# Optimization experiments

Measured on AMD Instinct MI355X. Metric: run time of the kernel, lower is better.

Reference implementation:

```python
import jax, jax.numpy as jnp
import numpy as np

# Hyperparameters (must match init_kwargs)
B, S, D = 1, 4096, 1024
H, DK, DV = 16, 64, 64
G, W, R = 1, 23, 8          # global, window, random tokens
KSEL = 1 + R + W            # selected keys per non-global query


def setup_inputs() -> dict:
    key = jax.random.key(0)
    ks = jax.random.split(key, 8)
    scale = 0.02
    Q = jax.random.normal(ks[0], (B, S, D), dtype=jnp.float32)
    K = jax.random.normal(ks[1], (B, S, D), dtype=jnp.float32)
    V = jax.random.normal(ks[2], (B, S, D), dtype=jnp.float32)
    Wq = jax.random.normal(ks[3], (D, H * DK), dtype=jnp.float32) * scale
    Wk = jax.random.normal(ks[4], (D, H * DK), dtype=jnp.float32) * scale
    Wv = jax.random.normal(ks[5], (D, H * DV), dtype=jnp.float32) * scale
    Wo = jax.random.normal(ks[6], (H * DV, D), dtype=jnp.float32) * scale
    # BigBird-style index table: [global(=token 0), random, sliding window]
    n_ng = S - 2 * G
    base = jnp.arange(G, S - G)                                   # [n_ng]
    win = base[:, None] + jnp.arange(W)[None, :] - (W - 1) // 2   # [n_ng, W]
    win = jnp.clip(win, 0, S - 1)
    rnd = jax.random.randint(ks[7], (n_ng, R), 1, S)              # [n_ng, R]
    glb = jnp.zeros((n_ng, 1), dtype=jnp.int64)
    idx = jnp.concatenate([glb, rnd.astype(jnp.int64), win.astype(jnp.int64)], axis=1)  # [n_ng, KSEL]
    return {"Q": Q, "K": K, "V": V, "Wq": Wq, "Wk": Wk, "Wv": Wv, "Wo": Wo, "idx": idx}


def reference(Q, K, V, Wq, Wk, Wv, Wo, idx):
    b, s, _ = Q.shape
    g = G
    # Projections, split heads: [B,H,S,d]
    q = (Q @ Wq).reshape(b, s, H, DK).transpose(0, 2, 1, 3)
    k = (K @ Wk).reshape(b, s, H, DK).transpose(0, 2, 1, 3)
    v = (V @ Wv).reshape(b, s, H, DV).transpose(0, 2, 1, 3)
    scale = 1.0 / jnp.sqrt(jnp.asarray(DK, dtype=q.dtype))

    # --- dense global-token path: first g and last g queries attend to all keys ---
    gidx = jnp.concatenate([jnp.arange(g), jnp.arange(s - g, s)])  # [2g]
    q_g = q[:, :, gidx, :]                                          # [B,H,2g,dk]
    logits_g = jnp.einsum('bhgd,bhnd->bhgn', q_g, k) * scale
    prob_g = jax.nn.softmax(logits_g, axis=-1)
    out_g = jnp.einsum('bhgn,bhnd->bhgd', prob_g, v)                # [B,H,2g,dv]

    # --- sparse gather path for the remaining queries ---
    q_ng = q[:, :, g:s - g, :]                                      # [B,H,n_ng,dk]
    k_sel = k[:, :, idx, :]                                         # [B,H,n_ng,KSEL,dk]
    v_sel = v[:, :, idx, :]                                         # [B,H,n_ng,KSEL,dv]
    logits = jnp.einsum('bhnd,bhnkd->bhnk', q_ng, k_sel) * scale
    prob = jax.nn.softmax(logits, axis=-1)
    out_ng = jnp.einsum('bhnk,bhnkd->bhnd', prob, v_sel)            # [B,H,n_ng,dv]

    out = jnp.concatenate([out_g[:, :, :g], out_ng, out_g[:, :, g:]], axis=2)  # [B,H,S,dv]
    x = out.transpose(0, 2, 1, 3).reshape(b, s, H * DV)
    return x @ Wo
```

## Files before the change

### kernel.cpp

```cpp
#include <hip/hip_runtime.h>

typedef unsigned short u16;
typedef unsigned int u32;
typedef __bf16 bf16x8_t __attribute__((ext_vector_type(8)));
typedef float f32x4 __attribute__((ext_vector_type(4)));
typedef float f32x2 __attribute__((ext_vector_type(2)));
typedef u32 u32x4 __attribute__((ext_vector_type(4)));
typedef u16 u16x8 __attribute__((ext_vector_type(8)));

__device__ __forceinline__ float b2f(u16 u) {
  u32 x = ((u32)u) << 16; float f; __builtin_memcpy(&f, &x, 4); return f;
}
__device__ __forceinline__ u16 f2b(float f) {
  u32 x; __builtin_memcpy(&x, &f, 4);
  return (u16)((x + 0x8000u) >> 16);
}
__device__ __forceinline__ f32x2 up2(u32 w) {
  u32 lo = w << 16, hi = w & 0xffff0000u;
  float a, b; __builtin_memcpy(&a, &lo, 4); __builtin_memcpy(&b, &hi, 4);
  f32x2 r; r[0] = a; r[1] = b; return r;
}

__device__ __forceinline__ u16x8 ld8(const void* p, size_t off, int f32) {
  if (!f32) return *(const u16x8*)((const u16*)p + off);
  const u32* u = (const u32*)p + off;
  u32x4 a = *(const u32x4*)u;
  u32x4 b = *(const u32x4*)(u + 4);
  u16x8 r;
#pragma unroll
  for (int e = 0; e < 4; ++e) r[e] = (u16)((a[e] + 0x8000u) >> 16);
#pragma unroll
  for (int e = 0; e < 4; ++e) r[4 + e] = (u16)((b[e] + 0x8000u) >> 16);
  return r;
}

#if __has_builtin(__builtin_amdgcn_global_load_lds)
__device__ __forceinline__ void gl_lds16(const u16* g, u16* l, int lane) {
  (void)lane;
  __builtin_amdgcn_global_load_lds(
      (const __attribute__((address_space(1))) void*)g,
      (__attribute__((address_space(3))) void*)l, 16, 0, 0);
}
#else
__device__ __forceinline__ void gl_lds16(const u16* g, u16* l, int lane) {
  *(u16x8*)(l + lane * 8) = *(const u16x8*)g;
}
#endif

__device__ __forceinline__ int det_f32(const u32* qraw, int lane) {
  int c = 0;
#pragma unroll
  for (int p = 0; p < 8; ++p) {
    const int e = (qraw[p * 64 + lane] >> 7) & 0xFF;
    c += (e >= 100 && e <= 141);
  }
  for (int off = 32; off; off >>= 1) c += __shfl_xor(c, off);
  return c < 300;
}
__device__ __forceinline__ int det_i64(const int* iraw, int lane) {
  int nz = (lane < 16) ? (iraw[(lane + 1) * 32 + 1] != 0) : 0;
  return __ballot(nz) == 0ull;
}

__global__ __launch_bounds__(256) void prep(
    const void* Q, const void* K, const void* V,
    const void* W0, const void* W1, const void* W2, const void* W3,
    u16* d0, u16* d1, u16* d2, u16* d3,
    u16* Qb, u16* Kb, u16* Vb) {
  const int tx = threadIdx.x, ty = threadIdx.y;
  const int t = ty * 32 + tx;
  const int f32 = det_f32((const u32*)Q, t & 63);
  const int z = blockIdx.z;
  if (z >= 4) {
    if (!f32) return;
    const void* s; u16* d;
    switch (z - 4) {
      case 0: s = Q; d = Qb; break;
      case 1: s = K; d = Kb; break;
      default: s = V; d = Vb; break;
    }
    const size_t i = ((size_t)(blockIdx.y * 32 + blockIdx.x) * 256 + t) * 16;
    *(u16x8*)(d + i) = ld8(s, i, 1);
    *(u16x8*)(d + i + 8) = ld8(s, i + 8, 1);
    return;
  }
  const void* src; u16* dst;
  switch (z) {
    case 0: src = W0; dst = d0; break;
    case 1: src = W1; dst = d1; break;
    case 2: src = W2; dst = d2; break;
    default: src = W3; dst = d3; break;
  }
  __shared__ u16 tile[32][33];
  const int bx = blockIdx.x * 32, by = blockIdx.y * 32;
#pragma unroll
  for (int i = 0; i < 4; ++i) {
    const int off = (by + ty + i * 8) * 1024 + bx + tx;
    tile[ty + i * 8][tx] = f32 ? f2b(((const float*)src)[off]) : ((const u16*)src)[off];
  }
  __syncthreads();
#pragma unroll
  for (int i = 0; i < 4; ++i)
    dst[(bx + ty + i * 8) * 1024 + by + tx] = tile[tx][ty + i * 8];
}

template <int BM>
__device__ __forceinline__ void gemm_fast(const void* A, int a_f32,
                                          const u16* __restrict__ Bt,
                                          void* C, int c_f32) {
  constexpr int AI = BM / 64;
  __shared__ __align__(16) u16 As[BM * 32];
  __shared__ __align__(16) u16 Bs[128 * 32];
  const int t = threadIdx.x;
  const int lane = t & 63, w = t >> 6;
  const int bm = blockIdx.x * BM, bn = blockIdx.y * 128;
  const int lr = lane >> 2, lc = (lane & 3) * 8;
  const int wr = (w >> 1) * (BM / 2);
  const int wc = (w & 1) * 64;
  const int m16 = lane & 15, q4 = lane >> 4;
  f32x4 acc[BM / 32][4] = {};

  for (int k0 = 0; k0 < 1024; k0 += 32) {
    if (!a_f32) {
#pragma unroll
      for (int i = 0; i < AI; ++i)
        gl_lds16((const u16*)A + (size_t)(bm + w * 16 * AI + i * 16 + lr) * 1024 + k0 + lc,
                 &As[(w * 16 * AI + i * 16) * 32], lane);
    } else {
#pragma unroll
      for (int i = 0; i < AI; ++i)
        *(u16x8*)&As[(w * 16 * AI + i * 16 + lr) * 32 + lc] =
            ld8(A, (size_t)(bm + w * 16 * AI + i * 16 + lr) * 1024 + k0 + lc, 1);
    }
    gl_lds16(Bt + (size_t)(bn + w * 32 + lr) * 1024 + k0 + lc, &Bs[(w * 32) * 32], lane);
    gl_lds16(Bt + (size_t)(bn + w * 32 + 16 + lr) * 1024 + k0 + lc, &Bs[(w * 32 + 16) * 32], lane);
    __syncthreads();
    bf16x8_t af[BM / 32], bfr[4];
#pragma unroll
    for (int i = 0; i < BM / 32; ++i)
      af[i] = *(const bf16x8_t*)&As[(wr + i * 16 + m16) * 32 + q4 * 8];
#pragma unroll
    for (int j = 0; j < 4; ++j)
      bfr[j] = *(const bf16x8_t*)&Bs[(wc + j * 16 + m16) * 32 + q4 * 8];
#pragma unroll
    for (int i = 0; i < BM / 32; ++i)
#pragma unroll
      for (int j = 0; j < 4; ++j)
        acc[i][j] = __builtin_amdgcn_mfma_f32_16x16x32_bf16(af[i], bfr[j], acc[i][j], 0, 0, 0);
    __syncthreads();
  }
#pragma unroll
  for (int i = 0; i < BM / 32; ++i)
#pragma unroll
    for (int r = 0; r < 4; ++r) {
      const int row = bm + wr + i * 16 + q4 * 4 + r;
#pragma unroll
      for (int j = 0; j < 4; ++j) {
        const int col = bn + wc + j * 16 + m16;
        const float x = acc[i][j][r];
        if (c_f32) ((float*)C)[(size_t)row * 1024 + col] = x;
        else       ((u16*)C)[(size_t)row * 1024 + col] = f2b(x);
      }
    }
}

__global__ __launch_bounds__(256) void gemm_qkv(
    const void* Q, const void* K, const void* V,
    const u16* Qb, const u16* Kb, const u16* Vb,
    const u16* WqT, const u16* WkT, const u16* WvT,
    u16* q, u16* k, u16* v, int big) {
  const int f32 = det_f32((const u32*)Q, threadIdx.x & 63);
  const void* Araw; const u16* Ab; const u16* Bt; u16* Cp;
  switch (blockIdx.z) {
    case 0:  Araw = Q; Ab = Qb; Bt = WqT; Cp = q; break;
    case 1:  Araw = K; Ab = Kb; Bt = WkT; Cp = k; break;
    default: Araw = V; Ab = Vb; Bt = WvT; Cp = v; break;
  }
  if (big && f32) gemm_fast<128>(Ab, 0, Bt, Cp, 0);
  else            gemm_fast<128>(Araw, f32, Bt, Cp, 0);
}

__global__ __launch_bounds__(256) void gemm_out(
    const void* Qdet, const u16* A, const u16* WoT, void* C) {
  const int f32 = det_f32((const u32*)Qdet, threadIdx.x & 63);
  gemm_fast<64>(A, 0, WoT, C, f32);
}

__global__ __launch_bounds__(256) void attn(
    u16* qp, const u16* __restrict__ kp, const u16* __restrict__ vp,
    const int* __restrict__ idx, float* __restrict__ part) {
  const int t = threadIdx.x;
  __shared__ float ps[512];
  __shared__ int sidx[32];
  __shared__ float qh[64];
  __shared__ float lg[512];
  __shared__ float red[4];
  __shared__ float pvs[4][64];

  if (blockIdx.x < 256) {
    const int qi = blockIdx.x >> 7;
    const int h = (blockIdx.x >> 3) & 15;
    const int c = blockIdx.x & 7;
    const int s = qi ? 4095 : 0;
    if (t < 8) {
      u16x8 v = *(const u16x8*)(qp + (size_t)s * 1024 + h * 64 + t * 8);
#pragma unroll
      for (int e = 0; e < 8; ++e) qh[t * 8 + e] = b2f((u16)v[e]);
    }
    __syncthreads();
    float lv[2];
#pragma unroll
    for (int i = 0; i < 2; ++i) {
      const int n = c * 512 + t + i * 256;
      const u16* krow = kp + (size_t)n * 1024 + h * 64;
      float acc = 0.f;
#pragma unroll
      for (int cc = 0; cc < 8; ++cc) {
        u16x8 kv = *(const u16x8*)(krow + cc * 8);
#pragma unroll
        for (int e = 0; e < 8; ++e) acc += qh[cc * 8 + e] * b2f((u16)kv[e]);
      }
      lv[i] = acc * 0.125f;
    }
    float m2 = fmaxf(lv[0], lv[1]);
    for (int off = 32; off; off >>= 1) m2 = fmaxf(m2, __shfl_xor(m2, off));
    if ((t & 63) == 0) red[t >> 6] = m2;
    __syncthreads();
    const float gm = fmaxf(fmaxf(red[0], red[1]), fmaxf(red[2], red[3]));
    const float p0 = __expf(lv[0] - gm), p1 = __expf(lv[1] - gm);
    lg[t & 255] = p0;
    lg[t + 256] = p1;
    float sm = p0 + p1;
    for (int off = 32; off; off >>= 1) sm += __shfl_xor(sm, off);
    __syncthreads();
    if ((t & 63) == 0) red[t >> 6] = sm;
    __syncthreads();
    const float ssum = red[0] + red[1] + red[2] + red[3];
    const int d = t & 63, cc = t >> 6;
    float acc = 0.f;
    for (int i = 0; i < 128; ++i) {
      const int nl = cc * 128 + i;
      acc += lg[nl] * b2f(vp[(size_t)(c * 512 + nl) * 1024 + h * 64 + d]);
    }
    pvs[cc][d] = acc;
    __syncthreads();
    float* dst = part + ((size_t)(qi * 16 + h) * 8 + c) * 66;
    if (t == 0) { dst[0] = gm; dst[1] = ssum; }
    if (t < 64) dst[2 + t] = pvs[0][t] + pvs[1][t] + pvs[2][t] + pvs[3][t];
    return;
  }

  const int b = blockIdx.x - 256;
  int s0 = (b & 7) * 512 + (b >> 3);
  if (s0 >= 4094) s0 = 3583;
  const int s = s0 + 1;
  const int w = t >> 6, lane = t & 63;
  const int i64f = det_i64(idx, lane);
  const int jj = lane >> 3, dl = lane & 7;

  if (t >= 224) {
    const int j = t - 224;
    const size_t e = (size_t)(s - 1) * 32 + j;
    sidx[j] = i64f ? idx[2 * e] : idx[e];
  }

  f32x2 qreg[4][4];
#pragma unroll
  for (int hh = 0; hh < 4; ++hh) {
    const u32x4 qw = *(const u32x4*)(qp + (size_t)s * 1024 + (w * 4 + hh) * 64 + dl * 8);
#pragma unroll
    for (int c = 0; c < 4; ++c) qreg[hh][c] = up2(qw[c]);
  }
  __syncthreads();

#pragma unroll
  for (int p = 0; p < 16; ++p) {
    const int h = w * 4 + (p >> 2);
    const int j = (p & 3) * 8 + jj;
    const u32x4 kw = *(const u32x4*)(kp + (size_t)sidx[j] * 1024 + h * 64 + dl * 8);
    f32x2 a2 = {0.f, 0.f};
#pragma unroll
    for (int c = 0; c < 4; ++c)
      a2 = __builtin_elementwise_fma(up2(kw[c]), qreg[p >> 2][c], a2);
    float acc = a2[0] + a2[1];
    acc += __shfl_xor(acc, 1);
    acc += __shfl_xor(acc, 2);
    acc += __shfl_xor(acc, 4);
    if (dl == 0) ps[h * 32 + j] = acc * 0.125f;
  }
  __syncthreads();

  {
    const int h = t >> 4, jx = t & 15;
    const float v0 = ps[h * 32 + jx], v1 = ps[h * 32 + jx + 16];
    float mx = fmaxf(v0, v1);
    mx = fmaxf(mx, __shfl_xor(mx, 1));
    mx = fmaxf(mx, __shfl_xor(mx, 2));
    mx = fmaxf(mx, __shfl_xor(mx, 4));
    mx = fmaxf(mx, __shfl_xor(mx, 8));
    const float p0 = __expf(v0 - mx), p1 = __expf(v1 - mx);
    float sm = p0 + p1;
    sm += __shfl_xor(sm, 1);
    sm += __shfl_xor(sm, 2);
    sm += __shfl_xor(sm, 4);
    sm += __shfl_xor(sm, 8);
    const float r = 1.f / sm;
    ps[h * 32 + jx] = p0 * r;
    ps[h * 32 + jx + 16] = p1 * r;
  }
  __syncthreads();

  const int dc = lane & 7;
#pragma unroll
  for (int hp = 0; hp < 4; ++hp) {
    const int h = hp * 4 + w;
    f32x2 acc2[4] = {};
#pragma unroll
    for (int j0 = 0; j0 < 32; j0 += 8) {
      const int j = j0 + jj;
      const u32x4 vw = *(const u32x4*)(vp + (size_t)sidx[j] * 1024 + h * 64 + dc * 8);
      const float p = ps[h * 32 + j];
      const f32x2 pp = {p, p};
#pragma unroll
      for (int c = 0; c < 4; ++c)
        acc2[c] = __builtin_elementwise_fma(up2(vw[c]), pp, acc2[c]);
    }
#pragma unroll
    for (int c = 0; c < 4; ++c)
#pragma unroll
      for (int e = 0; e < 2; ++e) {
        acc2[c][e] += __shfl_xor(acc2[c][e], 8);
        acc2[c][e] += __shfl_xor(acc2[c][e], 16);
        acc2[c][e] += __shfl_xor(acc2[c][e], 32);
      }
    if (jj == 0) {
      u16x8 o;
#pragma unroll
      for (int c = 0; c < 4; ++c) {
        o[c * 2] = f2b(acc2[c][0]);
        o[c * 2 + 1] = f2b(acc2[c][1]);
      }
      *(u16x8*)(qp + (size_t)s * 1024 + h * 64 + dc * 8) = o;
    }
  }
}

__global__ void attn_glb_b(u16* __restrict__ qp, const float* __restrict__ part) {
  const int qi = blockIdx.x >> 4, h = blockIdx.x & 15;
  const int s = qi ? 4095 : 0;
  const int t = threadIdx.x;
  const float* p = part + ((size_t)(qi * 16 + h) * 8) * 66;
  float gm = -1e30f;
#pragma unroll
  for (int c = 0; c < 8; ++c) gm = fmaxf(gm, p[c * 66]);
  float S = 0.f, o = 0.f;
#pragma unroll
  for (int c = 0; c < 8; ++c) {
    const float w = __expf(p[c * 66] - gm);
    S += p[c * 66 + 1] * w;
    o += p[c * 66 + 2 + t] * w;
  }
  qp[(size_t)s * 1024 + h * 64 + t] = f2b(o / S);
}

extern "C" void kernel_launch(void* const* d_in, const int* in_sizes, int n_in,
                              void* d_out, int out_size, void* d_ws, size_t ws_size,
                              hipStream_t stream) {
  const void* Q  = d_in[0];
  const void* K  = d_in[1];
  const void* V  = d_in[2];
  const void* Wq = d_in[3];
  const void* Wk = d_in[4];
  const void* Wv = d_in[5];
  const void* Wo = d_in[6];
  const int* idx = (const int*)d_in[7];

  u16* WqT = (u16*)d_ws;
  u16* WkT = WqT + (1 << 20);
  u16* WvT = WkT + (1 << 20);
  u16* WoT = WvT + (1 << 20);
  u16* qp  = WoT + (1 << 20);
  u16* vp  = qp + (4 << 20);
  float* part = (float*)WkT;
  u16* kp = (u16*)d_out;
  u16* Qb = (u16*)((char*)d_ws + (24ull << 20) + 4096);
  u16* Kb = Qb + (4 << 20);
  u16* Vb = Kb + (4 << 20);
  const bool big = ws_size >= (48ull << 20) + 8192;

  prep<<<dim3(32, 32, big ? 7 : 4), dim3(32, 8), 0, stream>>>(
      Q, K, V, Wq, Wk, Wv, Wo, WqT, WkT, WvT, WoT, Qb, Kb, Vb);
  gemm_qkv<<<dim3(32, 8, 3), 256, 0, stream>>>(
      Q, K, V, Qb, Kb, Vb, WqT, WkT, WvT, qp, kp, vp, big ? 1 : 0);
  attn<<<4350, 256, 0, stream>>>(qp, kp, vp, idx, part);
  attn_glb_b<<<32, 64, 0, stream>>>(qp, part);
  gemm_out<<<dim3(64, 8), 256, 0, stream>>>(Q, qp, WoT, d_out);
}
```

Baseline: 225.0 us.

## Restructure attention kernel to wave-local work without shared memory or block barriers

The sparse-query path now keeps the gathered indices, logits and softmax probabilities in registers. Indices are broadcast with wave shuffles, which removes all LDS staging and __syncthreads calls. The global-token path is re-split so each wave handles 128 keys of one head with vectorized 16-byte K/V loads, replacing per-element V loads and block reductions. The partial-result layout grows to 32 chunks of 72 floats, and the combine kernel changes to match. The larger partial buffer must fit in the workspace, and the combine step now has more partial chunks to read.

```diff
diff --git a/kernel.cpp b/kernel.cpp
--- a/kernel.cpp
+++ b/kernel.cpp
@@ -190,63 +190,73 @@
     u16* qp, const u16* __restrict__ kp, const u16* __restrict__ vp,
     const int* __restrict__ idx, float* __restrict__ part) {
   const int t = threadIdx.x;
-  __shared__ float ps[512];
-  __shared__ int sidx[32];
-  __shared__ float qh[64];
-  __shared__ float lg[512];
-  __shared__ float red[4];
-  __shared__ float pvs[4][64];
+  const int w = t >> 6, lane = t & 63;
+  const int jj = lane >> 3, dl = lane & 7;
 
   if (blockIdx.x < 256) {
-    const int qi = blockIdx.x >> 7;
-    const int h = (blockIdx.x >> 3) & 15;
-    const int c = blockIdx.x & 7;
+    const int gw = blockIdx.x * 4 + w;
+    const int qi = gw >> 9, h = (gw >> 5) & 15, c = gw & 31;
     const int s = qi ? 4095 : 0;
-    if (t < 8) {
-      u16x8 v = *(const u16x8*)(qp + (size_t)s * 1024 + h * 64 + t * 8);
-#pragma unroll
-      for (int e = 0; e < 8; ++e) qh[t * 8 + e] = b2f((u16)v[e]);
-    }
-    __syncthreads();
-    float lv[2];
-#pragma unroll
-    for (int i = 0; i < 2; ++i) {
-      const int n = c * 512 + t + i * 256;
-      const u16* krow = kp + (size_t)n * 1024 + h * 64;
-      float acc = 0.f;
-#pragma unroll
-      for (int cc = 0; cc < 8; ++cc) {
-        u16x8 kv = *(const u16x8*)(krow + cc * 8);
-#pragma unroll
-        for (int e = 0; e < 8; ++e) acc += qh[cc * 8 + e] * b2f((u16)kv[e]);
-      }
-      lv[i] = acc * 0.125f;
-    }
-    float m2 = fmaxf(lv[0], lv[1]);
-    for (int off = 32; off; off >>= 1) m2 = fmaxf(m2, __shfl_xor(m2, off));
-    if ((t & 63) == 0) red[t >> 6] = m2;
-    __syncthreads();
-    const float gm = fmaxf(fmaxf(red[0], red[1]), fmaxf(red[2], red[3]));
-    const float p0 = __expf(lv[0] - gm), p1 = __expf(lv[1] - gm);
-    lg[t & 255] = p0;
-    lg[t + 256] = p1;
-    float sm = p0 + p1;
-    for (int off = 32; off; off >>= 1) sm += __shfl_xor(sm, off);
-    __syncthreads();
-    if ((t & 63) == 0) red[t >> 6] = sm;
-    __syncthreads();
-    const float ssum = red[0] + red[1] + red[2] + red[3];
-    const int d = t & 63, cc = t >> 6;
-    float acc = 0.f;
-    for (int i = 0; i < 128; ++i) {
-      const int nl = cc * 128 + i;
-      acc += lg[nl] * b2f(vp[(size_t)(c * 512 + nl) * 1024 + h * 64 + d]);
-    }
-    pvs[cc][d] = acc;
-    __syncthreads();
-    float* dst = part + ((size_t)(qi * 16 + h) * 8 + c) * 66;
-    if (t == 0) { dst[0] = gm; dst[1] = ssum; }
-    if (t < 64) dst[2 + t] = pvs[0][t] + pvs[1][t] + pvs[2][t] + pvs[3][t];
+    f32x2 qreg[4];
+    {
+      const u32x4 qw = *(const u32x4*)(qp + (size_t)s * 1024 + h * 64 + dl * 8);
+#pragma unroll
+      for (int cc = 0; cc < 4; ++cc) qreg[cc] = up2(qw[cc]);
+    }
+    float lre[16];
+#pragma unroll
+    for (int p = 0; p < 16; ++p) {
+      const int n = c * 128 + p * 8 + jj;
+      const u32x4 kw = *(const u32x4*)(kp + (size_t)n * 1024 + h * 64 + dl * 8);
+      f32x2 a2 = {0.f, 0.f};
+#pragma unroll
+      for (int cc = 0; cc < 4; ++cc)
+        a2 = __builtin_elementwise_fma(up2(kw[cc]), qreg[cc], a2);
+      float acc = a2[0] + a2[1];
+      acc += __shfl_xor(acc, 1);
+      acc += __shfl_xor(acc, 2);
+      acc += __shfl_xor(acc, 4);
+      lre[p] = acc * 0.125f;
+    }
+    float mx = lre[0];
+#pragma unroll
+    for (int p = 1; p < 16; ++p) mx = fmaxf(mx, lre[p]);
+    mx = fmaxf(mx, __shfl_xor(mx, 8));
+    mx = fmaxf(mx, __shfl_xor(mx, 16));
+    mx = fmaxf(mx, __shfl_xor(mx, 32));
+    float sm = 0.f;
+#pragma unroll
+    for (int p = 0; p < 16; ++p) { lre[p] = __expf(lre[p] - mx); sm += lre[p]; }
+    sm += __shfl_xor(sm, 8);
+    sm += __shfl_xor(sm, 16);
+    sm += __shfl_xor(sm, 32);
+    f32x2 acc2[4] = {};
+#pragma unroll
+    for (int p = 0; p < 16; ++p) {
+      const int n = c * 128 + p * 8 + jj;
+      const u32x4 vw = *(const u32x4*)(vp + (size_t)n * 1024 + h * 64 + dl * 8);
+      const f32x2 pp = {lre[p], lre[p]};
+#pragma unroll
+      for (int cc = 0; cc < 4; ++cc)
+        acc2[cc] = __builtin_elementwise_fma(up2(vw[cc]), pp, acc2[cc]);
+    }
+#pragma unroll
+    for (int cc = 0; cc < 4; ++cc)
+#pragma unroll
+      for (int e = 0; e < 2; ++e) {
+        acc2[cc][e] += __shfl_xor(acc2[cc][e], 8);
+        acc2[cc][e] += __shfl_xor(acc2[cc][e], 16);
+        acc2[cc][e] += __shfl_xor(acc2[cc][e], 32);
+      }
+    float* dst = part + ((size_t)((qi * 16 + h) * 32 + c)) * 72;
+    if (lane == 0) { dst[0] = mx; dst[1] = sm; }
+    if (jj == 0) {
+#pragma unroll
+      for (int cc = 0; cc < 4; ++cc) {
+        dst[8 + dl * 8 + cc * 2] = acc2[cc][0];
+        dst[8 + dl * 8 + cc * 2 + 1] = acc2[cc][1];
+      }
+    }
     return;
   }
 
@@ -254,93 +264,83 @@
   int s0 = (b & 7) * 512 + (b >> 3);
   if (s0 >= 4094) s0 = 3583;
   const int s = s0 + 1;
-  const int w = t >> 6, lane = t & 63;
   const int i64f = det_i64(idx, lane);
-  const int jj = lane >> 3, dl = lane & 7;
-
-  if (t >= 224) {
-    const int j = t - 224;
-    const size_t e = (size_t)(s - 1) * 32 + j;
-    sidx[j] = i64f ? idx[2 * e] : idx[e];
-  }
-
+  int myidx;
+  {
+    const size_t e = (size_t)(s - 1) * 32 + (lane & 31);
+    myidx = i64f ? idx[2 * e] : idx[e];
+  }
+  const int h0 = w * 4;
   f32x2 qreg[4][4];
 #pragma unroll
   for (int hh = 0; hh < 4; ++hh) {
-    const u32x4 qw = *(const u32x4*)(qp + (size_t)s * 1024 + (w * 4 + hh) * 64 + dl * 8);
-#pragma unroll
-    for (int c = 0; c < 4; ++c) qreg[hh][c] = up2(qw[c]);
-  }
-  __syncthreads();
-
+    const u32x4 qw = *(const u32x4*)(qp + (size_t)s * 1024 + (h0 + hh) * 64 + dl * 8);
+#pragma unroll
+    for (int cc = 0; cc < 4; ++cc) qreg[hh][cc] = up2(qw[cc]);
+  }
+
+  float lre[4][4];
 #pragma unroll
   for (int p = 0; p < 16; ++p) {
-    const int h = w * 4 + (p >> 2);
-    const int j = (p & 3) * 8 + jj;
-    const u32x4 kw = *(const u32x4*)(kp + (size_t)sidx[j] * 1024 + h * 64 + dl * 8);
+    const int hh = p >> 2, q = p & 3;
+    const int row = __shfl(myidx, q * 8 + jj);
+    const u32x4 kw = *(const u32x4*)(kp + (size_t)row * 1024 + (h0 + hh) * 64 + dl * 8);
     f32x2 a2 = {0.f, 0.f};
 #pragma unroll
-    for (int c = 0; c < 4; ++c)
-      a2 = __builtin_elementwise_fma(up2(kw[c]), qreg[p >> 2][c], a2);
+    for (int cc = 0; cc < 4; ++cc)
+      a2 = __builtin_elementwise_fma(up2(kw[cc]), qreg[hh][cc], a2);
     float acc = a2[0] + a2[1];
     acc += __shfl_xor(acc, 1);
     acc += __shfl_xor(acc, 2);
     acc += __shfl_xor(acc, 4);
-    if (dl == 0) ps[h * 32 + j] = acc * 0.125f;
-  }
-  __syncthreads();
-
-  {
-    const int h = t >> 4, jx = t & 15;
-    const float v0 = ps[h * 32 + jx], v1 = ps[h * 32 + jx + 16];
-    float mx = fmaxf(v0, v1);
-    mx = fmaxf(mx, __shfl_xor(mx, 1));
-    mx = fmaxf(mx, __shfl_xor(mx, 2));
-    mx = fmaxf(mx, __shfl_xor(mx, 4));
+    lre[hh][q] = acc * 0.125f;
+  }
+
+#pragma unroll
+  for (int hh = 0; hh < 4; ++hh) {
+    float mx = fmaxf(fmaxf(lre[hh][0], lre[hh][1]), fmaxf(lre[hh][2], lre[hh][3]));
     mx = fmaxf(mx, __shfl_xor(mx, 8));
-    const float p0 = __expf(v0 - mx), p1 = __expf(v1 - mx);
-    float sm = p0 + p1;
-    sm += __shfl_xor(sm, 1);
-    sm += __shfl_xor(sm, 2);
-    sm += __shfl_xor(sm, 4);
+    mx = fmaxf(mx, __shfl_xor(mx, 16));
+    mx = fmaxf(mx, __shfl_xor(mx, 32));
+    float sm = 0.f;
+#pragma unroll
+    for (int q = 0; q < 4; ++q) { lre[hh][q] = __expf(lre[hh][q] - mx); sm += lre[hh][q]; }
     sm += __shfl_xor(sm, 8);
+    sm += __shfl_xor(sm, 16);
+    sm += __shfl_xor(sm, 32);
     const float r = 1.f / sm;
-    ps[h * 32 + jx] = p0 * r;
-    ps[h * 32 + jx + 16] = p1 * r;
-  }
-  __syncthreads();
-
-  const int dc = lane & 7;
-#pragma unroll
-  for (int hp = 0; hp < 4; ++hp) {
-    const int h = hp * 4 + w;
+#pragma unroll
+    for (int q = 0; q < 4; ++q) lre[hh][q] *= r;
+  }
+
+#pragma unroll
+  for (int hh = 0; hh < 4; ++hh) {
     f32x2 acc2[4] = {};
 #pragma unroll
-    for (int j0 = 0; j0 < 32; j0 += 8) {
-      const int j = j0 + jj;
-      const u32x4 vw = *(const u32x4*)(vp + (size_t)sidx[j] * 1024 + h * 64 + dc * 8);
-      const float p = ps[h * 32 + j];
-      const f32x2 pp = {p, p};
-#pragma unroll
-      for (int c = 0; c < 4; ++c)
-        acc2[c] = __builtin_elementwise_fma(up2(vw[c]), pp, acc2[c]);
-    }
-#pragma unroll
-    for (int c = 0; c < 4; ++c)
+    for (int q = 0; q < 4; ++q) {
+      const int row = __shfl(myidx, q * 8 + jj);
+      const u32x4 vw = *(const u32x4*)(vp + (size_t)row * 1024 + (h0 + hh) * 64 + dl * 8);
+      const f32x2 pp = {lre[hh][q], lre[hh][q]};
+#pragma unroll
+      for (int cc = 0; cc < 4; ++cc)
+        acc2[cc] = __builtin_elementwise_fma(up2(vw[cc]), pp, acc2[cc]);
+    }
+#pragma unroll
+    for (int cc = 0; cc < 4; ++cc)
 #pragma unroll
       for (int e = 0; e < 2; ++e) {
-        acc2[c][e] += __shfl_xor(acc2[c][e], 8);
-        acc2[c][e] += __shfl_xor(acc2[c][e], 16);
-        acc2[c][e] += __shfl_xor(acc2[c][e], 32);
+        acc2[cc][e] += __shfl_xor(acc2[cc][e], 8);
+        acc2[cc][e] += __shfl_xor(acc2[cc][e], 16);
+        acc2[cc][e] += __shfl_xor(acc2[cc][e], 32);
       }
     if (jj == 0) {
       u16x8 o;
 #pragma unroll
-      for (int c = 0; c < 4; ++c) {
-        o[c * 2] = f2b(acc2[c][0]);
-        o[c * 2 + 1] = f2b(acc2[c][1]);
-      }
-      *(u16x8*)(qp + (size_t)s * 1024 + h * 64 + dc * 8) = o;
+      for (int cc = 0; cc < 4; ++cc) {
+        o[cc * 2] = f2b(acc2[cc][0]);
+        o[cc * 2 + 1] = f2b(acc2[cc][1]);
+      }
+      *(u16x8*)(qp + (size_t)s * 1024 + (h0 + hh) * 64 + dl * 8) = o;
     }
   }
 }
@@ -349,16 +349,16 @@
   const int qi = blockIdx.x >> 4, h = blockIdx.x & 15;
   const int s = qi ? 4095 : 0;
   const int t = threadIdx.x;
-  const float* p = part + ((size_t)(qi * 16 + h) * 8) * 66;
+  const float* p = part + ((size_t)((qi * 16 + h) * 32)) * 72;
   float gm = -1e30f;
 #pragma unroll
-  for (int c = 0; c < 8; ++c) gm = fmaxf(gm, p[c * 66]);
+  for (int c = 0; c < 32; ++c) gm = fmaxf(gm, p[c * 72]);
   float S = 0.f, o = 0.f;
 #pragma unroll
-  for (int c = 0; c < 8; ++c) {
-    const float w = __expf(p[c * 66] - gm);
-    S += p[c * 66 + 1] * w;
-    o += p[c * 66 + 2 + t] * w;
+  for (int c = 0; c < 32; ++c) {
+    const float w = __expf(p[c * 72] - gm);
+    S += p[c * 72 + 1] * w;
+    o += p[c * 72 + 8 + t] * w;
   }
   qp[(size_t)s * 1024 + h * 64 + t] = f2b(o / S);
 }
```

New measurement: 213.0 us. -5.3%, faster.
